# Optimization experiments

Hardware: AMD Instinct MI355X
Metric: run time of the kernel (lower is better)

The kernel has to match this reference:

```python
import jax, jax.numpy as jnp
import numpy as np

IN_CH, OUT_CH, M1, M2 = 64, 64, 32, 32


def _powerlaw_psd_gaussian(key, exponent, n):
    """JAX port of colorednoise.powerlaw_psd_gaussian (fmin=0 default)."""
    f = jnp.fft.rfftfreq(n).astype(jnp.float32)  # [n//2+1]
    # fmin = max(0, 1/n); f[0]=0 is the only freq below it -> clamp to f[1]
    s_scale = jnp.where(f < 1.0 / n, f[1], f) ** (-exponent / 2.0)
    w = s_scale[1:]
    w = w.at[-1].multiply((1 + (n % 2)) / 2.0)  # Nyquist correction
    sigma = 2.0 * jnp.sqrt(jnp.sum(w * w)) / n
    kr, ki = jax.random.split(key)
    sr = jax.random.normal(kr, f.shape, jnp.float32) * s_scale
    si = jax.random.normal(ki, f.shape, jnp.float32) * s_scale
    if n % 2 == 0:
        si = si.at[-1].set(0.0)
        sr = sr.at[-1].multiply(jnp.sqrt(2.0))
    si = si.at[0].set(0.0)
    sr = sr.at[0].multiply(jnp.sqrt(2.0))
    return jnp.fft.irfft(sr + 1j * si, n=n) / sigma


def _compl_mul2d(t1, w, e_r, e_i, amp_r, amp_i, phi_r, phi_i, key):
    # Faithful to the torch code: stack over in-ch at dim=1 then sum dim=2
    # sums over the OUT channel axis => out[b,i,x,y] = t1[b,i,x,y]*sum_o w[i,o,x,y]
    out = t1 * jnp.sum(w, axis=1)[None]  # [B, IN_CH, M1, M2] complex
    b, c, m1, m2 = out.shape
    n = b * c * m1 * m2
    k1, k2 = jax.random.split(key)
    nr = jnp.roll(_powerlaw_psd_gaussian(k1, e_r, n), phi_r.astype(jnp.int32)) * amp_r
    ni = jnp.roll(_powerlaw_psd_gaussian(k2, e_i, n), phi_i.astype(jnp.int32)) * amp_i
    # original multiplies imag noise by amp_i twice (once in-place, once on reshape)
    noise = (nr + 1j * (ni * amp_i)).reshape(b, c, m1, m2)
    return out - noise


def _forward(x, w1, w2, exp_r, exp_i, nAmp_real, nAmp_imag, nPhase_real, nphase_imag):
    w1c = w1[..., 0] + 1j * w1[..., 1]  # [IN, OUT, M1, M2] complex64
    w2c = w2[..., 0] + 1j * w2[..., 1]
    e_r = jnp.median(exp_r)
    e_i = jnp.median(exp_i)
    amp_r = jnp.median(nAmp_real)
    amp_i = jnp.median(nAmp_imag)
    phi_r = jnp.median(nPhase_real)
    phi_i = jnp.median(nphase_imag)
    B, _, H, W = x.shape
    Wr = W // 2 + 1
    x_ft = jnp.fft.rfft2(x)  # [B, IN_CH, H, Wr]
    key = jax.random.key(42)
    kA, kB = jax.random.split(key)
    out_ft = jnp.zeros((B, OUT_CH, H, Wr), jnp.complex64)
    out_ft = out_ft.at[:, :, :M1, :M2].set(
        _compl_mul2d(x_ft[:, :, :M1, :M2], w1c, e_r, e_i, amp_r, amp_i, phi_r, phi_i, kA))
    out_ft = out_ft.at[:, :, -M1:, :M2].set(
        _compl_mul2d(x_ft[:, :, -M1:, :M2], w2c, e_r, e_i, amp_r, amp_i, phi_r, phi_i, kB))
    return jnp.fft.irfft2(out_ft, s=(H, W)).astype(jnp.float32)


def setup_inputs() -> dict:
    key = jax.random.key(0)
    ks = jax.random.split(key, 9)
    scale = 1.0 / (IN_CH * OUT_CH)
    return {
        "x": jax.random.normal(ks[0], (16, IN_CH, 256, 256), jnp.float32),
        "w1": scale * jax.random.uniform(ks[1], (IN_CH, OUT_CH, M1, M2, 2), jnp.float32),
        "w2": scale * jax.random.uniform(ks[2], (IN_CH, OUT_CH, M1, M2, 2), jnp.float32),
        "exp_r": jax.random.uniform(ks[3], (8,), jnp.float32),
        "exp_i": jax.random.uniform(ks[4], (8,), jnp.float32),
        "nAmp_real": jax.random.uniform(ks[5], (8,), jnp.float32),
        "nAmp_imag": jax.random.uniform(ks[6], (8,), jnp.float32),
        "nPhase_real": jax.random.normal(ks[7], (8,), jnp.float32),
        "nphase_imag": jax.random.normal(ks[8], (8,), jnp.float32),
    }


def reference(x, w1, w2, exp_r, exp_i, nAmp_real, nAmp_imag, nPhase_real, nphase_imag):
    return _forward(x, w1, w2, exp_r, exp_i, nAmp_real, nAmp_imag, nPhase_real, nphase_imag)
```

## Files before the change

### kernel.cpp

```cpp
#include <hip/hip_runtime.h>
#include <cstdint>

#define JPART 1
#define PART_XOR 1

constexpr uint32_t N20   = 1u << 20;
constexpr uint32_t NHALF = 1u << 19;
constexpr int SPT_STRIDE = 520;

struct Hdr {
  float e_r, e_i, amp_r, amp_i;
  int   phi_r, phi_i;
  float nhe_r, nhe_i;
  float scale_s[4];
};
struct KeyArgs { uint32_t k[8][2]; };

typedef __attribute__((ext_vector_type(8))) short short8;
typedef __attribute__((ext_vector_type(16))) float f32x16;

__device__ inline f32x16 zero16() {
  f32x16 v;
  #pragma unroll
  for (int i = 0; i < 16; ++i) v[i] = 0.f;
  return v;
}

__device__ inline unsigned short f2bf(float f) {
  uint32_t u = __float_as_uint(f);
  return (unsigned short)((u + 0x7fffu + ((u >> 16) & 1u)) >> 16);
}

__host__ __device__ inline void tf2x32(uint32_t k0, uint32_t k1, uint32_t x0, uint32_t x1,
                                       uint32_t& o0, uint32_t& o1) {
  const uint32_t ks0 = k0, ks1 = k1, ks2 = k0 ^ k1 ^ 0x1BD11BDAu;
  const uint32_t ks[3] = { ks0, ks1, ks2 };
  x0 += ks0; x1 += ks1;
  const int rot[2][4] = { {13,15,26,6}, {17,29,16,24} };
  for (int g = 0; g < 5; ++g) {
    const int* rr = rot[g & 1];
    for (int i = 0; i < 4; ++i) {
      x0 += x1;
      x1 = (x1 << rr[i]) | (x1 >> (32 - rr[i]));
      x1 ^= x0;
    }
    x0 += ks[(g + 1) % 3];
    x1 += ks[(g + 2) % 3] + (uint32_t)(g + 1);
  }
  o0 = x0; o1 = x1;
}

__device__ inline float erfinv_xla(float x) {
  float w = -log1pf(-x * x);
  float p;
  if (w < 5.0f) {
    w -= 2.5f;
    p = 2.81022636e-08f;
    p = fmaf(p, w, 3.43273939e-07f);
    p = fmaf(p, w, -3.5233877e-06f);
    p = fmaf(p, w, -4.39150654e-06f);
    p = fmaf(p, w, 0.00021858087f);
    p = fmaf(p, w, -0.00125372503f);
    p = fmaf(p, w, -0.00417768164f);
    p = fmaf(p, w, 0.246640727f);
    p = fmaf(p, w, 1.50140941f);
  } else {
    w = sqrtf(w) - 3.0f;
    p = -0.000200214257f;
    p = fmaf(p, w, 0.000100950558f);
    p = fmaf(p, w, 0.00134934322f);
    p = fmaf(p, w, -0.00367342844f);
    p = fmaf(p, w, 0.00573950773f);
    p = fmaf(p, w, -0.0076224613f);
    p = fmaf(p, w, 0.00943887047f);
    p = fmaf(p, w, 1.00167406f);
    p = fmaf(p, w, 2.83297682f);
  }
  return p * x;
}

__device__ inline float normal_from_bits(uint32_t bits) {
  uint32_t fb = (bits >> 9) | 0x3f800000u;
  float f = __uint_as_float(fb) - 1.0f;
  const float LO = -0.99999994f;
  float u = f * 2.0f + LO;
  u = fmaxf(LO, u);
  return 1.41421356f * erfinv_xla(u);
}

__device__ inline float sscale_f(uint32_t k, float nhe) {
  uint32_t kk = k ? k : 1u;
  return powf((float)kk * (1.0f / 1048576.0f), nhe);
}

__device__ inline float2 cmul(float2 a, float2 b) {
  return make_float2(a.x * b.x - a.y * b.y, a.x * b.y + a.y * b.x);
}
__device__ inline float2 wexp(float u) {
  float s, c; sincospif(2.0f * u, &s, &c); return make_float2(c, s);
}
__device__ inline float2 cadd(float2 a, float2 b){ return make_float2(a.x+b.x, a.y+b.y); }
__device__ inline float2 csub(float2 a, float2 b){ return make_float2(a.x-b.x, a.y-b.y); }
__device__ inline float2 cmuli(float2 a){ return make_float2(-a.y, a.x); }

__device__ inline int sA(int p) { return p ^ (((p >> 6) & 3) << 2) ^ ((p >> 8) & 3); }

__device__ inline void bfly(float2& y0, float2& y1, float2& y2, float2& y3, float2 W) {
  float2 a = cadd(y0, y2), b = csub(y0, y2);
  float2 c = cadd(y1, y3), d = cmuli(csub(y1, y3));
  float2 W2 = cmul(W, W), W3 = cmul(W2, W);
  y0 = cadd(a, c);
  y1 = cmul(cadd(b, d), W);
  y2 = cmul(csub(a, c), W2);
  y3 = cmul(csub(b, d), W3);
}

__device__ inline void fft1024_core(float2* r, float2* rc, float2* buf, int w) {
  #pragma unroll
  for (int e3 = 0; e3 < 4; ++e3) {
    float2 W = wexp((float)((e3 << 6) + w) * (1.0f / 1024.0f));
    bfly(r[e3], r[e3 + 4], r[e3 + 8], r[e3 + 12], W);
  }
  {
    float2 W = wexp((float)w * (1.0f / 256.0f));
    #pragma unroll
    for (int e4 = 0; e4 < 4; ++e4)
      bfly(r[(e4 << 2) + 0], r[(e4 << 2) + 1], r[(e4 << 2) + 2], r[(e4 << 2) + 3], W);
  }
  #pragma unroll
  for (int s = 0; s < 16; ++s) buf[sA((s << 6) + w)] = r[s];
  __syncthreads();
  {
    const int e0 = w & 3;
    const int pbase = ((w >> 4) << 8) + (((w >> 2) & 3) << 6) + e0;
    float2 rb[16];
    #pragma unroll
    for (int e2 = 0; e2 < 4; ++e2)
      #pragma unroll
      for (int e1 = 0; e1 < 4; ++e1)
        rb[(e2 << 2) + e1] = buf[sA(pbase + (e2 << 4) + (e1 << 2))];
    #pragma unroll
    for (int e1 = 0; e1 < 4; ++e1) {
      float2 W = wexp((float)((e1 << 2) + e0) * (1.0f / 64.0f));
      bfly(rb[e1], rb[e1 + 4], rb[e1 + 8], rb[e1 + 12], W);
    }
    {
      float2 W = wexp((float)e0 * (1.0f / 16.0f));
      #pragma unroll
      for (int e2 = 0; e2 < 4; ++e2)
        bfly(rb[(e2 << 2) + 0], rb[(e2 << 2) + 1], rb[(e2 << 2) + 2], rb[(e2 << 2) + 3], W);
    }
    #pragma unroll
    for (int e2 = 0; e2 < 4; ++e2)
      #pragma unroll
      for (int e1 = 0; e1 < 4; ++e1)
        buf[sA(pbase + (e2 << 4) + (e1 << 2))] = rb[(e2 << 2) + e1];
  }
  __syncthreads();
  {
    const int cbase = ((w >> 4) << 8) + (((w >> 2) & 3) << 6) + ((w & 3) << 4);
    #pragma unroll
    for (int e1 = 0; e1 < 4; ++e1)
      #pragma unroll
      for (int e0 = 0; e0 < 4; ++e0)
        rc[(e1 << 2) + e0] = buf[sA(cbase + (e1 << 2) + e0)];
    #pragma unroll
    for (int e1 = 0; e1 < 4; ++e1) {
      float2 x0 = rc[(e1 << 2)], x1 = rc[(e1 << 2) + 1], x2 = rc[(e1 << 2) + 2], x3 = rc[(e1 << 2) + 3];
      float2 a = cadd(x0, x2), b = csub(x0, x2);
      float2 c = cadd(x1, x3), d = cmuli(csub(x1, x3));
      rc[(e1 << 2)]     = cadd(a, c);
      rc[(e1 << 2) + 1] = cadd(b, d);
      rc[(e1 << 2) + 2] = csub(a, c);
      rc[(e1 << 2) + 3] = csub(b, d);
    }
  }
}

__device__ inline float med8_dev(const float* p) {
  float v[8];
  for (int i = 0; i < 8; ++i) v[i] = p[i];
  for (int i = 1; i < 8; ++i) { float key = v[i]; int j = i - 1;
    while (j >= 0 && v[j] > key) { v[j + 1] = v[j]; --j; } v[j + 1] = key; }
  return 0.5f * (v[3] + v[4]);
}

__global__ __launch_bounds__(256) void k_misc(Hdr* h,
    const float* er, const float* ei, const float* ar, const float* ai,
    const float* pr, const float* pim,
    const float* __restrict__ w1, const float* __restrict__ w2,
    float2* __restrict__ wsum,
    unsigned short* __restrict__ A_E, unsigned short* __restrict__ B2T,
    unsigned short* __restrict__ ET, unsigned short* __restrict__ Fc,
    unsigned short* __restrict__ Fs, unsigned short* __restrict__ Fns) {
  const int b = blockIdx.x;
  if (b == 960) {
    if (threadIdx.x) return;
    float mer = med8_dev(er), mei = med8_dev(ei);
    h->e_r = mer; h->e_i = mei;
    h->amp_r = med8_dev(ar); h->amp_i = med8_dev(ai);
    h->phi_r = (int)med8_dev(pr);
    h->phi_i = (int)med8_dev(pim);
    h->nhe_r = -0.5f * mer; h->nhe_i = -0.5f * mei;
    return;
  }
  if (b < 512) {
    int idx = b * 256 + threadIdx.x;
    int sel = idx >> 16, rem = idx & 65535;
    const float* w = sel ? w2 : w1;
    int c = rem >> 10, m1 = (rem >> 5) & 31, m2 = rem & 31;
    size_t base = (size_t)c * 131072 + (size_t)m1 * 64 + (size_t)m2 * 2;
    float sr = 0.f, si = 0.f;
    for (int oc = 0; oc < 64; ++oc) { sr += w[base + (size_t)oc * 2048]; si += w[base + (size_t)oc * 2048 + 1]; }
    wsum[idx] = make_float2(sr, si);
    return;
  }
  int t = (b - 512) * 256 + threadIdx.x;
  if (t < 32768) {
    int y = t >> 7, p = t & 127;
    int kyp = p & 63; int ky = (kyp < 32) ? kyp : kyp + 192;
    float s, c; sincospif(2.0f * (float)((ky * y) & 255) * (1.0f / 256.0f), &s, &c);
    A_E[t] = f2bf((p < 64) ? c : s);
  } else if (t < 49152) {
    int u = t - 32768;
    int x = u >> 6, j = u & 63, kx = j & 31;
    float s, c; sincospif(2.0f * (float)((kx * x) & 255) * (1.0f / 256.0f), &s, &c);
    float v = (j < 32) ? ((kx == 0) ? 1.0f : 2.0f * c)
                       : ((kx == 0) ? 0.0f : -2.0f * s);
    B2T[u] = f2bf(v * (1.0f / 65536.0f));
  } else if (t < 65536) {
    int u = t - 49152;
    int col = u >> 8, xx = u & 255; int kx = col & 31;
    float s, c; sincospif(2.0f * (float)((kx * xx) & 255) * (1.0f / 256.0f), &s, &c);
    ET[u] = f2bf((col < 32) ? c : -s);
  } else if (t < 114688) {
    int u = (t - 65536) & 16383;
    int which = (t - 65536) >> 14;
    int kyp = u >> 8, y = u & 255; int ky = (kyp < 32) ? kyp : kyp + 192;
    float s, c; sincospif(2.0f * (float)((ky * y) & 255) * (1.0f / 256.0f), &s, &c);
    if (which == 0) Fc[u] = f2bf(c);
    else if (which == 1) Fs[u] = f2bf(s);
    else Fns[u] = f2bf(-s);
  }
}

__global__ __launch_bounds__(256) void k_gen(const Hdr* __restrict__ h,
                                             float* __restrict__ partials,
                                             float4* __restrict__ spT, KeyArgs ka) {
  __shared__ float sr_[256], si_[256];
  const int b = blockIdx.x;
  if (b < 512) {
    const float nher = h->nhe_r, nhei = h->nhe_i;
    float sr = 0.f, si = 0.f;
    for (int j = 0; j < 4; ++j) {
      uint32_t k = (uint32_t)(b * 1024 + j * 256 + threadIdx.x) + 1u;
      float fk = (float)k * (1.0f / 1048576.0f);
      float wr = powf(fk, nher), wi = powf(fk, nhei);
      if (k == NHALF) { wr *= 0.5f; wi *= 0.5f; }
      sr += wr * wr; si += wi * wi;
    }
    sr_[threadIdx.x] = sr; si_[threadIdx.x] = si; __syncthreads();
    for (int off = 128; off > 0; off >>= 1) {
      if ((int)threadIdx.x < off) { sr_[threadIdx.x] += sr_[threadIdx.x + off];
                                    si_[threadIdx.x] += si_[threadIdx.x + off]; }
      __syncthreads();
    }
    if (!threadIdx.x) { partials[b * 2] = sr_[0]; partials[b * 2 + 1] = si_[0]; }
    return;
  }
  const int idx = b - 512;
  const int pair = idx >> 11;
  const int bx = idx & 2047;
  const int k1 = bx >> 1, chunk = bx & 1;
  const int k2 = (chunk << 8) + (int)threadIdx.x;
  const float nher = h->nhe_r, nhei = h->nhe_i;
  float4* row = spT + (size_t)pair * (1024 * SPT_STRIDE) + (size_t)k1 * SPT_STRIDE;
  const bool extra = (k1 == 0) && (chunk == 1) && (threadIdx.x == 255);
  const int niter = extra ? 2 : 1;
  for (int it = 0; it < niter; ++it) {
    const int kk2 = (it == 0) ? k2 : 512;
    const uint32_t i = (uint32_t)k1 + ((uint32_t)kk2 << 10);
    float vals[4];
    #pragma unroll
    for (int j = 0; j < 4; ++j) {
      const uint32_t K0 = ka.k[pair * 4 + j][0], K1 = ka.k[pair * 4 + j][1];
      uint32_t o0, o1; tf2x32(K0, K1, 0u, i, o0, o1);
#if PART_XOR
      uint32_t bits = o0 ^ o1;
#else
      uint32_t bits = o1;
#endif
      float nhe = (j < 2) ? nher : nhei;
      float v = normal_from_bits(bits) * sscale_f(i, nhe);
      if (i == 0u || i == NHALF) v = (j & 1) ? 0.0f : v * 1.41421356f;
      vals[j] = v;
    }
    row[kk2] = make_float4(vals[0], vals[1], vals[2], vals[3]);
  }
}

__global__ void k_sumw2_fin(Hdr* h, const float* partials) {
  if (threadIdx.x || blockIdx.x) return;
  float Sr = 0.f, Si = 0.f;
  for (int b = 0; b < 512; ++b) { Sr += partials[b * 2]; Si += partials[b * 2 + 1]; }
  float sig_r = 2.0f * sqrtf(Sr) * (1.0f / 1048576.0f);
  float sig_i = 2.0f * sqrtf(Si) * (1.0f / 1048576.0f);
  float s0 = h->amp_r / (sig_r * 1048576.0f);
  float s1 = (h->amp_i * h->amp_i) / (sig_i * 1048576.0f);
  h->scale_s[0] = s0; h->scale_s[1] = s1; h->scale_s[2] = s0; h->scale_s[3] = s1;
}

__global__ __launch_bounds__(256) void k_fft_s1(const float4* __restrict__ spT,
                                                float2* __restrict__ G) {
  __shared__ float2 buf4[4][1024];
  const int b = blockIdx.x;
  const int lin = (b & 7) * 64 + (b >> 3);
  const int pair = lin >> 8;
  const int g = threadIdx.x >> 6, w = threadIdx.x & 63;
  const int k1 = ((lin & 255) << 2) + g;
  const float4* sp = spT + (size_t)pair * (1024 * SPT_STRIDE);
  const int mrow = (1024 - k1) & 1023;

  float2 r[16], rc[16];
  #pragma unroll
  for (int s = 0; s < 16; ++s) {
    int k2 = (s << 6) + w;
    uint32_t k = (uint32_t)k1 + ((uint32_t)k2 << 10);
    float4 f; float2 z;
    if (k <= NHALF) {
      f = sp[(size_t)k1 * SPT_STRIDE + k2];
      z = make_float2(f.x - f.w, f.y + f.z);
    } else {
      int k2p = (k1 == 0) ? (1024 - k2) : (1023 - k2);
      f = sp[(size_t)mrow * SPT_STRIDE + k2p];
      z = make_float2(f.x + f.w, f.z - f.y);
    }
    r[s] = z;
  }
  fft1024_core(r, rc, buf4[g], w);
  float2* gp = G + ((size_t)pair << 20) + ((size_t)k1 << 10);
  const int klo = ((w & 3) << 4) + (((w >> 2) & 3) << 2) + (w >> 4);
  #pragma unroll
  for (int e1 = 0; e1 < 4; ++e1)
    #pragma unroll
    for (int e0 = 0; e0 < 4; ++e0) {
      int k = (e0 << 8) + (e1 << 6) + klo;
      float2 tw = wexp((float)(k * k1) * (1.0f / 1048576.0f));
      gp[k] = cmul(rc[(e1 << 2) + e0], tw);
    }
}

__global__ __launch_bounds__(256) void k_fft_s2(const float2* __restrict__ G,
                                                float2* __restrict__ noiseP,
                                                const Hdr* __restrict__ h) {
  __shared__ float2 buf4[4][1024];
  const int b = blockIdx.x;
  const int lin = (b & 7) * 64 + (b >> 3);
  const int pair = lin >> 8;
  const int g = threadIdx.x >> 6, w = threadIdx.x & 63;
  const int j2 = ((lin & 255) << 2) + g;

  float2 r[16], rc[16];
  const float2* gp = G + ((size_t)pair << 20) + (size_t)j2;
  #pragma unroll
  for (int s = 0; s < 16; ++s) r[s] = gp[(size_t)((s << 6) + w) << 10];
  fft1024_core(r, rc, buf4[g], w);
  const float scr = h->scale_s[0], sci = h->scale_s[1];
  float2* np_ = noiseP + ((size_t)pair << 20) + ((size_t)j2 << 10);
  const int klo = ((w & 3) << 4) + (((w >> 2) & 3) << 2) + (w >> 4);
  #pragma unroll
  for (int e1 = 0; e1 < 4; ++e1)
    #pragma unroll
    for (int e0 = 0; e0 < 4; ++e0) {
      int k = (e0 << 8) + (e1 << 6) + klo;
      np_[k] = make_float2(rc[(e1 << 2) + e0].x * scr, rc[(e1 << 2) + e0].y * sci);
    }
}

__global__ __launch_bounds__(256) void k_ntrans(const float2* __restrict__ noiseP,
                                                float* __restrict__ noiseL,
                                                const Hdr* __restrict__ h) {
  __shared__ float tr[64][65];
  __shared__ float ti[64][65];
  const int b = blockIdx.x;
  const int pair = b >> 8, tid = b & 255;
  const int R0 = (tid >> 4) << 6;
  const int C0 = (tid & 15) << 6;
  const int t = threadIdx.x;
  const int tx = t & 63, ty = t >> 6;
  const int phir = h->phi_r, phii = h->phi_i;
  const float2* src = noiseP + ((size_t)pair << 20);
  float* dstr = noiseL + ((size_t)(pair * 2) << 20);
  float* dsti = noiseL + ((size_t)(pair * 2 + 1) << 20);
  #pragma unroll
  for (int i = 0; i < 16; ++i) {
    int r = (i << 2) + ty;
    float2 v = src[(size_t)((R0 + r) << 10) + (size_t)(C0 + tx)];
    tr[r][tx] = v.x; ti[r][tx] = v.y;
  }
  __syncthreads();
  #pragma unroll
  for (int i = 0; i < 16; ++i) {
    int c = (i << 2) + ty;
    int n = ((C0 + c) << 10) + R0 + tx;
    dstr[(uint32_t)(n + phir) & (N20 - 1u)] = tr[tx][c];
    dsti[(uint32_t)(n + phii) & (N20 - 1u)] = ti[tx][c];
  }
}

__global__ __launch_bounds__(256, 2) void k_forward(const float* __restrict__ x,
    const float2* __restrict__ wsum, const float* __restrict__ noiseL,
    const unsigned short* __restrict__ ET, const unsigned short* __restrict__ Fc,
    const unsigned short* __restrict__ Fs, const unsigned short* __restrict__ Fns,
    float2* __restrict__ oftg) {
  __shared__ char lds[65536];
  char* X1T = lds + 32768;
  const int bc = blockIdx.x, t = threadIdx.x;
  const int c = bc & 63;
  const int l = t & 63, w = t >> 6, lr = l & 31, kg = l >> 5;
  const int rt = w >> 1, ct = w & 1;
  const float* xim = x + ((size_t)bc << 16);

  float4 pf[16];
  #pragma unroll
  for (int i = 0; i < 16; ++i) {
    int f4 = i * 256 + t;
    int r = f4 >> 6, c4 = f4 & 63;
    pf[i] = *(const float4*)(xim + (size_t)((r) << 8) + (c4 << 2));
  }

  #pragma unroll
  for (int yt = 0; yt < 4; ++yt) {
    __syncthreads();
    #pragma unroll
    for (int i = 0; i < 16; ++i) {
      int f4 = i * 256 + t;
      int r = f4 >> 6, c4 = f4 & 63;
      ushort4 b4; b4.x = f2bf(pf[i].x); b4.y = f2bf(pf[i].y);
      b4.z = f2bf(pf[i].z); b4.w = f2bf(pf[i].w);
      int byte = ((r << 9) + (c4 << 3)) ^ ((r & 7) << 4);
      *(ushort4*)(lds + byte) = b4;
    }
    __syncthreads();
    if (yt < 3) {
      #pragma unroll
      for (int i = 0; i < 16; ++i) {
        int f4 = i * 256 + t;
        int r = f4 >> 6, c4 = f4 & 63;
        pf[i] = *(const float4*)(xim + (size_t)((((yt + 1) << 6) + r) << 8) + (c4 << 2));
      }
    }
    f32x16 a1 = zero16();
    const int arow = (rt << 5) + lr;
    const int bcol = (ct << 5) + lr;
    #pragma unroll
    for (int s = 0; s < 16; ++s) {
      short8 af = *(const short8*)(lds + (((arow << 9) + (s << 5) + (kg << 4)) ^ ((arow & 7) << 4)));
      short8 bf = *(const short8*)(ET + (bcol << 8) + (s << 4) + (kg << 3));
      a1 = __builtin_amdgcn_mfma_f32_32x32x16_bf16(af, bf, a1, 0, 0, 0);
    }
    #pragma unroll
    for (int r4 = 0; r4 < 4; ++r4) {
      int y0 = (yt << 6) + (rt << 5) + (r4 << 3) + (kg << 2);
      ushort4 p4;
      p4.x = f2bf(a1[r4 * 4 + 0]); p4.y = f2bf(a1[r4 * 4 + 1]);
      p4.z = f2bf(a1[r4 * 4 + 2]); p4.w = f2bf(a1[r4 * 4 + 3]);
      int byte = ((bcol << 9) + (y0 << 1)) ^ ((bcol & 7) << 4);
      *(ushort4*)(X1T + byte) = p4;
    }
  }
  __syncthreads();

  const int re_im = w >> 1, kt = w & 1;
  const unsigned short* A1p = re_im ? Fns : Fs;
  const int b0row = (re_im ? 32 : 0) + lr;
  const int b1row = (re_im ? 0 : 32) + lr;
  const int a2row = (kt << 5) + lr;
  f32x16 a2 = zero16();
  #pragma unroll
  for (int s = 0; s < 16; ++s) {
    short8 a0f = *(const short8*)(Fc  + (a2row << 8) + (s << 4) + (kg << 3));
    short8 a1f = *(const short8*)(A1p + (a2row << 8) + (s << 4) + (kg << 3));
    short8 b0f = *(const short8*)(X1T + (((b0row << 9) + (s << 5) + (kg << 4)) ^ ((b0row & 7) << 4)));
    short8 b1f = *(const short8*)(X1T + (((b1row << 9) + (s << 5) + (kg << 4)) ^ ((b1row & 7) << 4)));
    a2 = __builtin_amdgcn_mfma_f32_32x32x16_bf16(a0f, b0f, a2, 0, 0, 0);
    a2 = __builtin_amdgcn_mfma_f32_32x32x16_bf16(a1f, b1f, a2, 0, 0, 0);
  }
  float* Osm = (float*)(lds + (re_im << 13));
  #pragma unroll
  for (int i = 0; i < 16; ++i) {
    int row = (kt << 5) + (i & 3) + ((i >> 2) << 3) + (kg << 2);
    Osm[(row << 5) + lr] = a2[i];
  }
  __syncthreads();

  const float* Ore = (const float*)lds;
  const float* Oim = (const float*)(lds + 8192);
  #pragma unroll
  for (int r = 0; r < 8; ++r) {
    int idx = (r << 8) + t;
    int kyp = idx >> 5, kx = idx & 31;
    int sel = kyp >> 5, m1 = kyp & 31;
    float2 av = make_float2(Ore[idx], Oim[idx]);
    float2 wv = wsum[((size_t)sel << 16) + (size_t)(((c << 5) | m1) << 5) + (size_t)kx];
    float2 v;
    v.x = av.x * wv.x - av.y * wv.y;
    v.y = av.x * wv.y + av.y * wv.x;
    uint32_t p = ((uint32_t)((bc << 5) | m1) << 5) | (uint32_t)kx;
    const float* nlr = noiseL + ((size_t)(sel ? 2 : 0) << 20);
    const float* nli = noiseL + ((size_t)(sel ? 3 : 1) << 20);
    v.x -= nlr[p];
    v.y -= nli[p];
    oftg[((size_t)bc << 11) + (size_t)idx] = v;
  }
}

__global__ __launch_bounds__(256) void k_inverse(const float2* __restrict__ oftg,
    const unsigned short* __restrict__ A_E, const unsigned short* __restrict__ B2T,
    float* __restrict__ out) {
  __shared__ char smem[32768];

  const int bc = blockIdx.x, t = threadIdx.x;
  const int l = t & 63, w = t >> 6, lr = l & 31, kg = l >> 5;

  {
    const float* ob = (const float*)(oftg + ((size_t)bc << 11));
    #pragma unroll
    for (int i = 0; i < 32; ++i) {
      int idx = t + (i << 8);
      int p = idx >> 6, j = idx & 63;
      int kyp = p & 63;
      float v;
      if (p < 64) v = (j < 32) ? ob[(kyp << 6) + (j << 1)]
                               : ob[(kyp << 6) + ((j - 32) << 1) + 1];
      else        v = (j < 32) ? -ob[(kyp << 6) + (j << 1) + 1]
                               : ob[(kyp << 6) + ((j - 32) << 1)];
      int byte = ((j << 8) + (p << 1)) ^ ((j & 7) << 4);
      *(unsigned short*)(smem + byte) = f2bf(v);
    }
  }
  __syncthreads();

  f32x16 acc[2][2];
  acc[0][0] = zero16(); acc[0][1] = zero16(); acc[1][0] = zero16(); acc[1][1] = zero16();
  #pragma unroll
  for (int s = 0; s < 8; ++s) {
    short8 af[2], bf[2];
    #pragma unroll
    for (int rt = 0; rt < 2; ++rt) {
      int row = (w << 6) + (rt << 5) + lr;
      af[rt] = *(const short8*)(A_E + (row << 7) + (s << 4) + (kg << 3));
    }
    #pragma unroll
    for (int ct = 0; ct < 2; ++ct) {
      int j = (ct << 5) + lr;
      int byte = ((j << 8) + (s << 5) + (kg << 4)) ^ ((j & 7) << 4);
      bf[ct] = *(const short8*)(smem + byte);
    }
    #pragma unroll
    for (int rt = 0; rt < 2; ++rt)
      #pragma unroll
      for (int ct = 0; ct < 2; ++ct)
        acc[rt][ct] = __builtin_amdgcn_mfma_f32_32x32x16_bf16(af[rt], bf[ct], acc[rt][ct], 0, 0, 0);
  }
  __syncthreads();

  #pragma unroll
  for (int rt = 0; rt < 2; ++rt)
    #pragma unroll
    for (int ct = 0; ct < 2; ++ct)
      #pragma unroll
      for (int r = 0; r < 16; ++r) {
        int row = (w << 6) + (rt << 5) + (r & 3) + (((r >> 2) & 3) << 3) + (kg << 2);
        int col = (ct << 5) + lr;
        int byte = ((row << 7) + (col << 1)) ^ ((row & 7) << 4);
        *(unsigned short*)(smem + byte) = f2bf(acc[rt][ct][r]);
      }
  __syncthreads();

  short8 ta[2][4];
  #pragma unroll
  for (int rt = 0; rt < 2; ++rt)
    #pragma unroll
    for (int ks = 0; ks < 4; ++ks) {
      int row = (w << 6) + (rt << 5) + lr;
      int byte = ((row << 7) + (ks << 5) + (kg << 4)) ^ ((row & 7) << 4);
      ta[rt][ks] = *(const short8*)(smem + byte);
    }
  float* op = out + ((size_t)bc << 16);
  #pragma unroll
  for (int cc = 0; cc < 4; ++cc) {
    short8 b2[2][4];
    #pragma unroll
    for (int cx = 0; cx < 2; ++cx)
      #pragma unroll
      for (int ks = 0; ks < 4; ++ks) {
        int xx = (cc << 6) + (cx << 5) + lr;
        b2[cx][ks] = *(const short8*)(B2T + (xx << 6) + (ks << 4) + (kg << 3));
      }
    f32x16 a2[2][2];
    a2[0][0] = zero16(); a2[0][1] = zero16(); a2[1][0] = zero16(); a2[1][1] = zero16();
    #pragma unroll
    for (int ks = 0; ks < 4; ++ks)
      #pragma unroll
      for (int rt = 0; rt < 2; ++rt)
        #pragma unroll
        for (int cx = 0; cx < 2; ++cx)
          a2[rt][cx] = __builtin_amdgcn_mfma_f32_32x32x16_bf16(ta[rt][ks], b2[cx][ks], a2[rt][cx], 0, 0, 0);
    #pragma unroll
    for (int rt = 0; rt < 2; ++rt)
      #pragma unroll
      for (int cx = 0; cx < 2; ++cx)
        #pragma unroll
        for (int r = 0; r < 16; ++r) {
          int row = (w << 6) + (rt << 5) + (r & 3) + (((r >> 2) & 3) << 3) + (kg << 2);
          int xx = (cc << 6) + (cx << 5) + lr;
          op[(row << 8) + xx] = a2[rt][cx][r];
        }
  }
}

extern "C" void kernel_launch(void* const* d_in, const int* in_sizes, int n_in,
                              void* d_out, int out_size, void* d_ws, size_t ws_size,
                              hipStream_t stream) {
  (void)in_sizes; (void)n_in; (void)out_size; (void)ws_size;
  const float* x   = (const float*)d_in[0];
  const float* w1  = (const float*)d_in[1];
  const float* w2  = (const float*)d_in[2];
  const float* er  = (const float*)d_in[3];
  const float* ei  = (const float*)d_in[4];
  const float* ar  = (const float*)d_in[5];
  const float* ai  = (const float*)d_in[6];
  const float* pr  = (const float*)d_in[7];
  const float* pim = (const float*)d_in[8];
  float* out = (float*)d_out;

  char* ws = (char*)d_ws;
  Hdr*    hdr      = (Hdr*)ws;
  float*  partials = (float*)(ws + 0x1000);
  float2* wsum     = (float2*)(ws + 0x10000);
  unsigned short* A_E = (unsigned short*)(ws + 0x130000);
  unsigned short* B2T = (unsigned short*)(ws + 0x140000);
  unsigned short* ET  = (unsigned short*)(ws + 0x148000);
  unsigned short* Fc  = (unsigned short*)(ws + 0x150000);
  unsigned short* Fs  = (unsigned short*)(ws + 0x158000);
  unsigned short* Fns = (unsigned short*)(ws + 0x160000);
  float4* spT      = (float4*)(ws + 0x200000);
  float2* G        = (float2*)(ws + 0x1400000);
  float2* oft      = (float2*)(ws + 0x1400000);
  float2* noiseP   = (float2*)(ws + 0x2400000);
  float*  noiseL   = (float*)(ws + 0x3400000);

  auto splitk = [](const uint32_t k[2], uint32_t a[2], uint32_t b[2]) {
#if JPART
    tf2x32(k[0], k[1], 0u, 0u, a[0], a[1]);
    tf2x32(k[0], k[1], 0u, 1u, b[0], b[1]);
#else
    uint32_t r0[2], r1[2];
    tf2x32(k[0], k[1], 0u, 2u, r0[0], r0[1]);
    tf2x32(k[0], k[1], 1u, 3u, r1[0], r1[1]);
    a[0] = r0[0]; a[1] = r1[0]; b[0] = r0[1]; b[1] = r1[1];
#endif
  };
  uint32_t root[2] = { 0u, 42u };
  uint32_t kA[2], kB[2], k1A[2], k2A[2], k1B[2], k2B[2];
  splitk(root, kA, kB);
  splitk(kA, k1A, k2A);
  splitk(kB, k1B, k2B);
  KeyArgs ka;
  splitk(k1A, ka.k[0], ka.k[1]);
  splitk(k2A, ka.k[2], ka.k[3]);
  splitk(k1B, ka.k[4], ka.k[5]);
  splitk(k2B, ka.k[6], ka.k[7]);

  hipLaunchKernelGGL(k_misc,      dim3(961),      dim3(256), 0, stream, hdr, er, ei, ar, ai, pr, pim,
                     w1, w2, wsum, A_E, B2T, ET, Fc, Fs, Fns);
  hipLaunchKernelGGL(k_gen,       dim3(4608),     dim3(256), 0, stream, hdr, partials, spT, ka);
  hipLaunchKernelGGL(k_sumw2_fin, dim3(1),        dim3(64),  0, stream, hdr, partials);
  hipLaunchKernelGGL(k_fft_s1,    dim3(512),      dim3(256), 0, stream, spT, G);
  hipLaunchKernelGGL(k_fft_s2,    dim3(512),      dim3(256), 0, stream, G, noiseP, hdr);
  hipLaunchKernelGGL(k_ntrans,    dim3(512),      dim3(256), 0, stream, noiseP, noiseL, hdr);
  hipLaunchKernelGGL(k_forward,   dim3(1024),     dim3(256), 0, stream, x, wsum, noiseL, ET, Fc, Fs, Fns, oft);
  hipLaunchKernelGGL(k_inverse,   dim3(1024),     dim3(256), 0, stream, oft, A_E, B2T, out);
}
```

Measured before the change: 267.8 us.

## Coalesce FFT stage-1 writes via LDS transpose and split forward kernel in two

Result: slower. 275.3 us (+2.8%).

```diff
diff --git a/kernel.cpp b/kernel.cpp
--- a/kernel.cpp
+++ b/kernel.cpp
@@ -317,7 +317,8 @@
   const int lin = (b & 7) * 64 + (b >> 3);
   const int pair = lin >> 8;
   const int g = threadIdx.x >> 6, w = threadIdx.x & 63;
-  const int k1 = ((lin & 255) << 2) + g;
+  const int k1b = (lin & 255) << 2;
+  const int k1 = k1b + g;
   const float4* sp = spT + (size_t)pair * (1024 * SPT_STRIDE);
   const int mrow = (1024 - k1) & 1023;
 
@@ -338,7 +339,6 @@
     r[s] = z;
   }
   fft1024_core(r, rc, buf4[g], w);
-  float2* gp = G + ((size_t)pair << 20) + ((size_t)k1 << 10);
   const int klo = ((w & 3) << 4) + (((w >> 2) & 3) << 2) + (w >> 4);
   #pragma unroll
   for (int e1 = 0; e1 < 4; ++e1)
@@ -346,8 +346,17 @@
     for (int e0 = 0; e0 < 4; ++e0) {
       int k = (e0 << 8) + (e1 << 6) + klo;
       float2 tw = wexp((float)(k * k1) * (1.0f / 1048576.0f));
-      gp[k] = cmul(rc[(e1 << 2) + e0], tw);
-    }
+      buf4[g][sA(k)] = cmul(rc[(e1 << 2) + e0], tw);
+    }
+  __syncthreads();
+  const int t = threadIdx.x;
+  float2* gp = G + ((size_t)pair << 20) + (size_t)k1b;
+  const int k1off = t & 3;
+  #pragma unroll
+  for (int it = 0; it < 16; ++it) {
+    int j2 = (it << 6) + (t >> 2);
+    gp[((size_t)j2 << 10) + k1off] = buf4[k1off][sA(j2)];
+  }
 }
 
 __global__ __launch_bounds__(256) void k_fft_s2(const float2* __restrict__ G,
@@ -361,9 +370,9 @@
   const int j2 = ((lin & 255) << 2) + g;
 
   float2 r[16], rc[16];
-  const float2* gp = G + ((size_t)pair << 20) + (size_t)j2;
-  #pragma unroll
-  for (int s = 0; s < 16; ++s) r[s] = gp[(size_t)((s << 6) + w) << 10];
+  const float2* gp = G + ((size_t)pair << 20) + ((size_t)j2 << 10);
+  #pragma unroll
+  for (int s = 0; s < 16; ++s) r[s] = gp[(s << 6) + w];
   fft1024_core(r, rc, buf4[g], w);
   const float scr = h->scale_s[0], sci = h->scale_s[1];
   float2* np_ = noiseP + ((size_t)pair << 20) + ((size_t)j2 << 10);
@@ -408,18 +417,14 @@
   }
 }
 
-__global__ __launch_bounds__(256, 2) void k_forward(const float* __restrict__ x,
-    const float2* __restrict__ wsum, const float* __restrict__ noiseL,
-    const unsigned short* __restrict__ ET, const unsigned short* __restrict__ Fc,
-    const unsigned short* __restrict__ Fs, const unsigned short* __restrict__ Fns,
-    float2* __restrict__ oftg) {
-  __shared__ char lds[65536];
-  char* X1T = lds + 32768;
+__global__ __launch_bounds__(256) void k_fwd1(const float* __restrict__ x,
+    const unsigned short* __restrict__ ET, unsigned short* __restrict__ X1g) {
+  __shared__ char lds[32768];
   const int bc = blockIdx.x, t = threadIdx.x;
-  const int c = bc & 63;
   const int l = t & 63, w = t >> 6, lr = l & 31, kg = l >> 5;
   const int rt = w >> 1, ct = w & 1;
   const float* xim = x + ((size_t)bc << 16);
+  unsigned short* xg = X1g + ((size_t)bc << 14);
 
   float4 pf[16];
   #pragma unroll
@@ -460,13 +465,37 @@
       a1 = __builtin_amdgcn_mfma_f32_32x32x16_bf16(af, bf, a1, 0, 0, 0);
     }
     #pragma unroll
-    for (int r4 = 0; r4 < 4; ++r4) {
-      int y0 = (yt << 6) + (rt << 5) + (r4 << 3) + (kg << 2);
-      ushort4 p4;
-      p4.x = f2bf(a1[r4 * 4 + 0]); p4.y = f2bf(a1[r4 * 4 + 1]);
-      p4.z = f2bf(a1[r4 * 4 + 2]); p4.w = f2bf(a1[r4 * 4 + 3]);
-      int byte = ((bcol << 9) + (y0 << 1)) ^ ((bcol & 7) << 4);
-      *(ushort4*)(X1T + byte) = p4;
+    for (int i = 0; i < 16; ++i) {
+      int y = (yt << 6) + (rt << 5) + ((i >> 2) << 3) + (kg << 2) + (i & 3);
+      xg[(y << 6) + bcol] = f2bf(a1[i]);
+    }
+  }
+}
+
+__global__ __launch_bounds__(256) void k_fwd2(const unsigned short* __restrict__ X1g,
+    const float2* __restrict__ wsum, const float* __restrict__ noiseL,
+    const unsigned short* __restrict__ Fc, const unsigned short* __restrict__ Fs,
+    const unsigned short* __restrict__ Fns, float2* __restrict__ oftg) {
+  __shared__ char X1T[32768];
+  const int bc = blockIdx.x, t = threadIdx.x;
+  const int c = bc & 63;
+  const int l = t & 63, w = t >> 6, lr = l & 31, kg = l >> 5;
+
+  {
+    const unsigned short* xg = X1g + ((size_t)bc << 14);
+    #pragma unroll
+    for (int i = 0; i < 8; ++i) {
+      int e = i * 2048 + t * 8;
+      int y = e >> 6, col0 = e & 63;
+      ushort4 v0 = *(const ushort4*)(xg + e);
+      ushort4 v1 = *(const ushort4*)(xg + e + 4);
+      unsigned short vv[8] = { v0.x, v0.y, v0.z, v0.w, v1.x, v1.y, v1.z, v1.w };
+      #pragma unroll
+      for (int j = 0; j < 8; ++j) {
+        int col = col0 + j;
+        int byte = ((col << 9) + (y << 1)) ^ ((col & 7) << 4);
+        *(unsigned short*)(X1T + byte) = vv[j];
+      }
     }
   }
   __syncthreads();
@@ -486,7 +515,8 @@
     a2 = __builtin_amdgcn_mfma_f32_32x32x16_bf16(a0f, b0f, a2, 0, 0, 0);
     a2 = __builtin_amdgcn_mfma_f32_32x32x16_bf16(a1f, b1f, a2, 0, 0, 0);
   }
-  float* Osm = (float*)(lds + (re_im << 13));
+  __syncthreads();
+  float* Osm = (float*)(X1T + (re_im << 13));
   #pragma unroll
   for (int i = 0; i < 16; ++i) {
     int row = (kt << 5) + (i & 3) + ((i >> 2) << 3) + (kg << 2);
@@ -494,8 +524,8 @@
   }
   __syncthreads();
 
-  const float* Ore = (const float*)lds;
-  const float* Oim = (const float*)(lds + 8192);
+  const float* Ore = (const float*)X1T;
+  const float* Oim = (const float*)(X1T + 8192);
   #pragma unroll
   for (int r = 0; r < 8; ++r) {
     int idx = (r << 8) + t;
@@ -647,7 +677,8 @@
   unsigned short* Fns = (unsigned short*)(ws + 0x160000);
   float4* spT      = (float4*)(ws + 0x200000);
   float2* G        = (float2*)(ws + 0x1400000);
-  float2* oft      = (float2*)(ws + 0x1400000);
+  unsigned short* X1g = (unsigned short*)(ws + 0x200000);
+  float2* oft      = (float2*)(ws + 0x2400000);
   float2* noiseP   = (float2*)(ws + 0x2400000);
   float*  noiseL   = (float*)(ws + 0x3400000);
 
@@ -680,6 +711,7 @@
   hipLaunchKernelGGL(k_fft_s1,    dim3(512),      dim3(256), 0, stream, spT, G);
   hipLaunchKernelGGL(k_fft_s2,    dim3(512),      dim3(256), 0, stream, G, noiseP, hdr);
   hipLaunchKernelGGL(k_ntrans,    dim3(512),      dim3(256), 0, stream, noiseP, noiseL, hdr);
-  hipLaunchKernelGGL(k_forward,   dim3(1024),     dim3(256), 0, stream, x, wsum, noiseL, ET, Fc, Fs, Fns, oft);
+  hipLaunchKernelGGL(k_fwd1,      dim3(1024),     dim3(256), 0, stream, x, ET, X1g);
+  hipLaunchKernelGGL(k_fwd2,      dim3(1024),     dim3(256), 0, stream, X1g, wsum, noiseL, Fc, Fs, Fns, oft);
   hipLaunchKernelGGL(k_inverse,   dim3(1024),     dim3(256), 0, stream, oft, A_E, B2T, out);
 }
```
